# Kernel optimization log

Measured on AMD Instinct MI355X. Metric: run time of the kernel, lower is better.

Reference implementation:

```python
import jax, jax.numpy as jnp
import numpy as np

H = W = 256          # full-res feature map (2h x 2w)
WIN = 16             # window size
STRIDE = 2           # shifted-window stride
HEADS = 8
DIM_HEAD = 64
INNER = HEADS * DIM_HEAD
DIM = 128
KEEP = 50            # min(int(0.7*(256//16)**2), 50)
IOU_THR = 0.2


def _make_windows():
    xs = np.arange(0, W - WIN + 1, STRIDE)
    ys = np.arange(0, H - WIN + 1, STRIDE)
    gx, gy = np.meshgrid(xs, ys)
    return np.stack([gx.ravel(), gy.ravel(), gx.ravel() + WIN - 1, gy.ravel() + WIN - 1], axis=1)

_WIN_NP = _make_windows()          # [M,4] = (x1,y1,x2,y2), M = 121*121 = 14641
BOXES = jnp.asarray(_WIN_NP, dtype=jnp.float32)
SXY = jnp.asarray(_WIN_NP[:, :2], dtype=jnp.int32)   # integer (sx, sy) origins

# torchvision roi_align (spatial_scale=1, sampling_ratio->ceil(15/16)=1, aligned=False):
_off = (np.arange(WIN) + 0.5) * (WIN - 1.0) / WIN
LO = jnp.asarray(np.floor(_off).astype(np.int32))      # low integer index, in [0,14]
FR = jnp.asarray((_off - np.floor(_off)).astype(np.float32))


def _nms_keep(scores):
    """Greedy NMS over the fixed window grid; returns top-KEEP kept indices."""
    x1, y1, x2, y2 = BOXES[:, 0], BOXES[:, 1], BOXES[:, 2], BOXES[:, 3]
    area = (x2 - x1) * (y2 - y1)

    def body(k, carry):
        live, keep = carry
        idx = jnp.argmax(jnp.where(live, scores, -jnp.inf))
        bb = BOXES[idx]
        iw = jnp.clip(jnp.minimum(x2, bb[2]) - jnp.maximum(x1, bb[0]), 0.0)
        ih = jnp.clip(jnp.minimum(y2, bb[3]) - jnp.maximum(y1, bb[1]), 0.0)
        inter = iw * ih
        iou = inter / (area + area[idx] - inter)
        live = live & (iou <= IOU_THR)
        return live, keep.at[k].set(idx.astype(jnp.int32))

    _, keep = jax.lax.fori_loop(
        0, KEEP, body,
        (jnp.ones(BOXES.shape[0], bool), jnp.zeros(KEEP, jnp.int32)))
    return keep


def _forward(x, prob, fix_w, w_qkv, w_out, b_out):
    b = prob.shape[0]
    d = x.shape[-1]
    # entropy map at half res
    entropy = -jnp.sum(prob * jnp.log2(prob + 1e-10), axis=1)          # [b,128,128]
    # FixCNN: 8x8 ones-init conv, VALID -> [b,1,121,121]; normalized window score
    score = jax.lax.conv_general_dilated(
        entropy[:, None], fix_w, (1, 1), 'VALID',
        dimension_numbers=('NCHW', 'OIHW', 'NCHW'))
    score = score.reshape(b, -1) / float((WIN // 2) * (WIN // 2))      # [b,14641]

    keep = jax.lax.stop_gradient(jax.vmap(_nms_keep)(score))           # [b,KEEP]
    sx = SXY[keep][..., 0]                                             # [b,KEEP]
    sy = SXY[keep][..., 1]

    x2d = x.reshape(b, H, W, d)   # token n = h*W + w (channels-last layout)
    ar = jnp.arange(WIN)

    def gather_one(xi, syi, sxi):  # xi [H,W,d]
        R = syi[:, None, None] + ar[None, :, None]
        C = sxi[:, None, None] + ar[None, None, :]
        return xi[R, C]

    crops = jax.vmap(gather_one)(x2d, sy, sx)                          # [b,K,16,16,d]

    # roi_align bilinear sampling with fixed fractional grid
    c00 = crops[:, :, LO[:, None], LO[None, :]]
    c01 = crops[:, :, LO[:, None], LO[None, :] + 1]
    c10 = crops[:, :, LO[:, None] + 1, LO[None, :]]
    c11 = crops[:, :, LO[:, None] + 1, LO[None, :] + 1]
    fy = FR[:, None, None]
    fx = FR[None, :, None]
    win = ((1 - fy) * (1 - fx) * c00 + (1 - fy) * fx * c01
           + fy * (1 - fx) * c10 + fy * fx * c11)                      # [b,K,16,16,d]

    toks = win.reshape(b * KEEP, WIN * WIN, d)                         # [m,256,d]
    qkv = toks @ w_qkv.T                                               # [m,256,3*INNER]
    q, k_, v = jnp.split(qkv, 3, axis=-1)

    def to_heads(t):
        return t.reshape(t.shape[0], t.shape[1], HEADS, DIM_HEAD).transpose(0, 2, 1, 3)

    q, k_, v = to_heads(q), to_heads(k_), to_heads(v)
    attn = jax.nn.softmax(jnp.einsum('mhnd,mhkd->mhnk', q, k_) * (DIM_HEAD ** -0.5), axis=-1)
    out = jnp.einsum('mhnk,mhkd->mhnd', attn, v)
    out = out.transpose(0, 2, 1, 3).reshape(b * KEEP, WIN * WIN, INNER)
    out = out @ w_out.T + b_out                                        # [m,256,d]

    # overlap scatter-add + count normalization
    out2d = out.reshape(b, KEEP, WIN, WIN, d)
    bidx = jnp.arange(b)[:, None, None, None]
    Y = sy[:, :, None, None] + ar[None, None, :, None]
    X = sx[:, :, None, None] + ar[None, None, None, :]
    acc = jnp.zeros((b, H, W, d), x.dtype).at[bidx, Y, X].add(out2d)
    cnt = jnp.zeros((b, H, W), x.dtype).at[bidx, Y, X].add(1.0)
    outx = (acc / (cnt[..., None] + 1e-10)).reshape(b, H * W, d)
    return x + outx


def setup_inputs() -> dict:
    key = jax.random.key(0)
    ks = jax.random.split(key, 4)
    b = 4
    x = jax.random.normal(ks[0], (b, H * W, DIM), dtype=jnp.float32)
    prob = jax.random.uniform(ks[1], (b, 2, H // 2, W // 2), dtype=jnp.float32)
    fix_w = jnp.ones((1, 1, WIN // 2, WIN // 2), dtype=jnp.float32)
    w_qkv = jax.random.normal(ks[2], (3 * INNER, DIM), dtype=jnp.float32) * 0.02
    w_out = jax.random.normal(ks[3], (DIM, INNER), dtype=jnp.float32) * 0.02
    b_out = jnp.zeros((DIM,), dtype=jnp.float32)
    return {"x": x, "prob": prob, "fix_w": fix_w, "w_qkv": w_qkv, "w_out": w_out, "b_out": b_out}


def reference(x, prob, fix_w, w_qkv, w_out, b_out):
    return _forward(x, prob, fix_w, w_qkv, w_out, b_out)
```

## Files before the change

kernel.cpp:

```cpp
#include <hip/hip_runtime.h>
#include <math.h>

#define NB 4
#define NWIN 121
#define NBOX (NWIN*NWIN)
#define NKEEP 50
#define HWD 256
#define DIM 128
#define HEADS 8
#define NTOK 256
#define NWTOT (NB*NKEEP)
#define SCPAD 15616

#define OFF_ENT   0
#define OFF_SCORE 65536
#define OFF_KEEP  128128
#define OFF_WQKV  128256
#define OFF_WOUT  226560
#define OFF_TOKBF 259328
#define OFF_PO    3536128
#define WS_FLOATS 6812928

#define KPAD 76
#define VPAD 268

typedef __attribute__((ext_vector_type(8))) short short8;
typedef __attribute__((ext_vector_type(4))) short short4v;
typedef __attribute__((ext_vector_type(4))) float f32x4;

static __device__ __forceinline__ unsigned short f2bf(float f) {
  union { float f; unsigned u; } v; v.f = f;
  unsigned r = (v.u + 0x7fffu + ((v.u >> 16) & 1u)) >> 16;
  return (unsigned short)r;
}
static __device__ __forceinline__ short4v pk4(f32x4 a) {
  short4v r;
  r[0] = (short)f2bf(a[0]); r[1] = (short)f2bf(a[1]);
  r[2] = (short)f2bf(a[2]); r[3] = (short)f2bf(a[3]);
  return r;
}
static __device__ __forceinline__ short8 ld8_lds(const unsigned short* p) {
  short4v a = *(const short4v*)p;
  short4v b = *(const short4v*)(p + 4);
  short8 r;
  r[0]=a[0]; r[1]=a[1]; r[2]=a[2]; r[3]=a[3];
  r[4]=b[0]; r[5]=b[1]; r[6]=b[2]; r[7]=b[3];
  return r;
}
static __device__ __forceinline__ short8 ld8_g(const unsigned short* p) {
  return *(const short8*)p;
}

template<int CTRL>
static __device__ __forceinline__ float dppmax(float v) {
  union { float f; int i; } a, r; a.f = v;
  r.i = __builtin_amdgcn_update_dpp(a.i, a.i, CTRL, 0xf, 0xf, false);
  return fmaxf(v, r.f);
}
static __device__ __forceinline__ float wavemax(float v) {
  v = dppmax<0x111>(v); v = dppmax<0x112>(v);
  v = dppmax<0x114>(v); v = dppmax<0x118>(v);
  v = dppmax<0x142>(v); v = dppmax<0x143>(v);
  union { float f; int i; } gi, gm; gi.f = v;
  gm.i = __builtin_amdgcn_readlane(gi.i, 63);
  return gm.f;
}

__global__ void k_entropy(const float* __restrict__ prob, float* __restrict__ ent) {
  int idx = blockIdx.x * 256 + threadIdx.x;
  int b = idx >> 14, p = idx & 16383;
  float p0 = prob[(size_t)(b * 2) * 16384 + p];
  float p1 = prob[(size_t)(b * 2 + 1) * 16384 + p];
  ent[idx] = -(p0 * log2f(p0 + 1e-10f) + p1 * log2f(p1 + 1e-10f));
}

__global__ void k_score(const float* __restrict__ ent, const float* __restrict__ fw,
                        float* __restrict__ scp) {
  int gid = blockIdx.x * 256 + threadIdx.x;
  if (gid >= NB * SCPAD) return;
  int b = gid / SCPAD, idx = gid % SCPAD;
  int r = idx >> 7, c = idx & 127;
  float s = -INFINITY;
  if (r < NWIN && c < NWIN) {
    const float* e = ent + b * 16384 + r * 128 + c;
    float a = 0.f;
#pragma unroll
    for (int rr = 0; rr < 8; ++rr)
#pragma unroll
      for (int cc = 0; cc < 8; ++cc)
        a += e[rr * 128 + cc] * fw[rr * 8 + cc];
    s = a * (1.0f / 64.0f);
  }
  scp[b * SCPAD + (r << 7) + (c ^ ((r & 7) << 2))] = s;
}

__global__ void k_nms(const float* __restrict__ scp, int* __restrict__ keep) {
  __shared__ float sc[SCPAD];
  int b = blockIdx.x, l = threadIdx.x;
  const float* src = scp + b * SCPAD;
  for (int cb = 0; cb < 64; cb += 8) {
    f32x4 t[8];
#pragma unroll
    for (int i = 0; i < 8; ++i) {
      int idx = (cb + i) * 256 + l * 4;
      if (idx < SCPAD) t[i] = *(const f32x4*)&src[idx];
    }
#pragma unroll
    for (int i = 0; i < 8; ++i) {
      int idx = (cb + i) * 256 + l * 4;
      if (idx < SCPAD) *(f32x4*)&sc[idx] = t[i];
    }
  }
  float M0 = -INFINITY, M1 = -INFINITY; int C0 = 0, C1 = 0;
#pragma unroll
  for (int slot = 0; slot < 2; ++slot) {
    int r = l + slot * 64;
    if (slot == 1 && r >= NWIN) break;
    int r7 = (r & 7) << 2, rbase = r << 7;
    float bv0=-INFINITY,bv1=-INFINITY,bv2=-INFINITY,bv3=-INFINITY;
    int bc0=0,bc1=0,bc2=0,bc3=0;
    for (int lb = 0; lb < 32; ++lb) {
      f32x4 v = *(const f32x4*)&sc[rbase + ((lb << 2) ^ r7)];
      int c0 = lb << 2;
      if (v[0] > bv0) { bv0 = v[0]; bc0 = c0; }
      if (v[1] > bv1) { bv1 = v[1]; bc1 = c0 + 1; }
      if (v[2] > bv2) { bv2 = v[2]; bc2 = c0 + 2; }
      if (v[3] > bv3) { bv3 = v[3]; bc3 = c0 + 3; }
    }
    float bv = bv0; int bc = bc0;
    if (bv1 > bv || (bv1 == bv && bc1 < bc)) { bv = bv1; bc = bc1; }
    if (bv2 > bv || (bv2 == bv && bc2 < bc)) { bv = bv2; bc = bc2; }
    if (bv3 > bv || (bv3 == bv && bc3 < bc)) { bv = bv3; bc = bc3; }
    if (slot == 0) { M0 = bv; C0 = bc; } else { M1 = bv; C1 = bc; }
  }

  for (int k = 0; k < NKEEP; ++k) {
    float gmax = wavemax(fmaxf(M0, M1));
    unsigned long long b0 = __ballot(M0 == gmax);
    unsigned long long b1 = __ballot(M1 == gmax);
    int R;
    if (b0) R = __ffsll((unsigned long long)b0) - 1;
    else    R = 64 + __ffsll((unsigned long long)b1) - 1;
    int Cc = (R < 64) ? __builtin_amdgcn_readlane(C0, R)
                      : __builtin_amdgcn_readlane(C1, R - 64);
    if (l == 0) {
      keep[(b * NKEEP + k) * 2 + 0] = 2 * R;
      keep[(b * NKEEP + k) * 2 + 1] = 2 * Cc;
    }
    bool kill0 = false, kill1 = false;
    {
      int dy = l - R, ady = dy < 0 ? -dy : dy;
      if (ady <= 4) {
        int ih = 15 - 2 * ady;
#pragma unroll
        for (int dx = -4; dx <= 4; ++dx) {
          int adx = dx < 0 ? -dx : dx;
          if ((15 - 2 * adx) * ih > 75) {
            int cc = Cc + dx;
            if ((unsigned)cc < (unsigned)NWIN)
              sc[(l << 7) + (cc ^ ((l & 7) << 2))] = -INFINITY;
          }
        }
        int adx = C0 - Cc; adx = adx < 0 ? -adx : adx;
        kill0 = (adx <= 4) && ((15 - 2 * adx) * ih > 75);
      }
    }
    if (l + 64 < NWIN) {
      int r1 = l + 64;
      int dy = r1 - R, ady = dy < 0 ? -dy : dy;
      if (ady <= 4) {
        int ih = 15 - 2 * ady;
#pragma unroll
        for (int dx = -4; dx <= 4; ++dx) {
          int adx = dx < 0 ? -dx : dx;
          if ((15 - 2 * adx) * ih > 75) {
            int cc = Cc + dx;
            if ((unsigned)cc < (unsigned)NWIN)
              sc[(r1 << 7) + (cc ^ ((r1 & 7) << 2))] = -INFINITY;
          }
        }
        int adx = C1 - Cc; adx = adx < 0 ? -adx : adx;
        kill1 = (adx <= 4) && ((15 - 2 * adx) * ih > 75);
      }
    }
    unsigned long long need0 = __ballot(kill0);
    unsigned long long need1 = __ballot(kill1);
    while (need0 | need1) {
      int rr;
      if (need0) { rr = __ffsll((unsigned long long)need0) - 1; need0 &= need0 - 1; }
      else       { rr = __ffsll((unsigned long long)need1) - 1 + 64; need1 &= need1 - 1; }
      int r7 = (rr & 7) << 2, rbase = rr << 7;
      float v0 = sc[rbase + (l ^ r7)];
      float v1 = sc[rbase + ((l + 64) ^ r7)];
      float rmax = wavemax(fmaxf(v0, v1));
      unsigned long long e0 = __ballot(v0 == rmax);
      unsigned long long e1 = __ballot(v1 == rmax);
      int bc;
      if (e0) bc = __ffsll((unsigned long long)e0) - 1;
      else    bc = 64 + __ffsll((unsigned long long)e1) - 1;
      if (l == (rr & 63)) {
        if (rr >= 64) { M1 = rmax; C1 = bc; }
        else          { M0 = rmax; C0 = bc; }
      }
    }
  }
}

__global__ void k_wcvt(const float* __restrict__ wqkv, const float* __restrict__ wout,
                       unsigned short* __restrict__ wqkv_bf, unsigned short* __restrict__ wout_bf) {
  int i = blockIdx.x * 256 + threadIdx.x;
  if (i < 196608) wqkv_bf[i] = f2bf(wqkv[i]);
  int j = i - 196608;
  if (j >= 0 && j < 65536) wout_bf[j] = f2bf(wout[j]);
}

__global__ void k_toks(const float* __restrict__ x, const int* __restrict__ keep,
                       unsigned short* __restrict__ tokbf) {
  int w = blockIdx.x;
  int b = w / NKEEP;
  int sy = keep[w * 2 + 0], sx = keep[w * 2 + 1];
  int tid = threadIdx.x;
  int ch = tid & 127, th = tid >> 7;
  const float* xb = x + (size_t)b * 65536 * DIM;
  for (int it = 0; it < 128; ++it) {
    int tk = it * 2 + th;
    int i = tk >> 4, j = tk & 15;
    float offy = (i + 0.5f) * 0.9375f;
    float offx = (j + 0.5f) * 0.9375f;
    int li = (int)offy, lj = (int)offx;
    float fy = offy - (float)li, fx = offx - (float)lj;
    const float* p = xb + ((size_t)((sy + li) * HWD + (sx + lj))) * DIM + ch;
    float v00 = p[0], v01 = p[DIM], v10 = p[HWD * DIM], v11 = p[HWD * DIM + DIM];
    float w00 = (1.f - fy) * (1.f - fx), w01 = (1.f - fy) * fx;
    float w10 = fy * (1.f - fx), w11 = fy * fx;
    tokbf[((size_t)w * NTOK + tk) * DIM + ch] = f2bf(w00 * v00 + w01 * v01 + w10 * v10 + w11 * v11);
  }
}

__global__ __launch_bounds__(512, 2) void k_attn(
    const unsigned short* __restrict__ tokbf,
    const unsigned short* __restrict__ wqkv,
    const unsigned short* __restrict__ wout,
    unsigned short* __restrict__ po) {
  __shared__ __align__(16) char smem[112128];
  unsigned short* Klds = (unsigned short*)smem;
  unsigned short* VT   = (unsigned short*)(smem + 38912);
  const int tid = threadIdx.x;
  const int wv = tid >> 6, ln = tid & 63;
  const int lo = ln & 15, hi = ln >> 4;
  const int win = blockIdx.x;
  unsigned short* QP = (unsigned short*)(smem + 73216 + wv * 4864);
  const unsigned short* tw = tokbf + (size_t)win * NTOK * DIM;
  const int qrow = wv * 32;

  f32x4 pacc[8][2];
#pragma unroll
  for (int mf = 0; mf < 8; ++mf)
#pragma unroll
    for (int nf = 0; nf < 2; ++nf) pacc[mf][nf] = (f32x4){0.f,0.f,0.f,0.f};

  for (int h = 0; h < HEADS; ++h) {
    if (h) __syncthreads();

    {
      f32x4 kacc[4][2];
#pragma unroll
      for (int mf = 0; mf < 4; ++mf)
#pragma unroll
        for (int nf = 0; nf < 2; ++nf) kacc[mf][nf] = (f32x4){0.f,0.f,0.f,0.f};
#pragma unroll
      for (int kf = 0; kf < 4; ++kf) {
        short8 aw[4], bt[2];
#pragma unroll
        for (int mf = 0; mf < 4; ++mf)
          aw[mf] = ld8_g(wqkv + (size_t)(512 + h * 64 + mf * 16 + lo) * 128 + kf * 32 + hi * 8);
#pragma unroll
        for (int nf = 0; nf < 2; ++nf)
          bt[nf] = ld8_g(&tw[(qrow + nf * 16 + lo) * 128 + kf * 32 + hi * 8]);
#pragma unroll
        for (int mf = 0; mf < 4; ++mf)
#pragma unroll
          for (int nf = 0; nf < 2; ++nf)
            kacc[mf][nf] = __builtin_amdgcn_mfma_f32_16x16x32_bf16(aw[mf], bt[nf], kacc[mf][nf], 0, 0, 0);
      }
#pragma unroll
      for (int mf = 0; mf < 4; ++mf)
#pragma unroll
        for (int nf = 0; nf < 2; ++nf)
          *(short4v*)&Klds[(qrow + nf * 16 + lo) * KPAD + mf * 16 + hi * 4] = pk4(kacc[mf][nf]);
    }
    {
      f32x4 vacc[2][4];
#pragma unroll
      for (int mf = 0; mf < 2; ++mf)
#pragma unroll
        for (int nf = 0; nf < 4; ++nf) vacc[mf][nf] = (f32x4){0.f,0.f,0.f,0.f};
#pragma unroll
      for (int kf = 0; kf < 4; ++kf) {
        short8 at[2], bw[4];
#pragma unroll
        for (int mf = 0; mf < 2; ++mf)
          at[mf] = ld8_g(&tw[(qrow + mf * 16 + lo) * 128 + kf * 32 + hi * 8]);
#pragma unroll
        for (int nf = 0; nf < 4; ++nf)
          bw[nf] = ld8_g(wqkv + (size_t)(1024 + h * 64 + nf * 16 + lo) * 128 + kf * 32 + hi * 8);
#pragma unroll
        for (int mf = 0; mf < 2; ++mf)
#pragma unroll
          for (int nf = 0; nf < 4; ++nf)
            vacc[mf][nf] = __builtin_amdgcn_mfma_f32_16x16x32_bf16(at[mf], bw[nf], vacc[mf][nf], 0, 0, 0);
      }
#pragma unroll
      for (int mf = 0; mf < 2; ++mf)
#pragma unroll
        for (int nf = 0; nf < 4; ++nf)
          *(short4v*)&VT[(nf * 16 + lo) * VPAD + qrow + mf * 16 + hi * 4] = pk4(vacc[mf][nf]);
    }
    {
      f32x4 qacc[4][2];
#pragma unroll
      for (int mf = 0; mf < 4; ++mf)
#pragma unroll
        for (int nf = 0; nf < 2; ++nf) qacc[mf][nf] = (f32x4){0.f,0.f,0.f,0.f};
#pragma unroll
      for (int kf = 0; kf < 4; ++kf) {
        short8 aw[4], bt[2];
#pragma unroll
        for (int mf = 0; mf < 4; ++mf)
          aw[mf] = ld8_g(wqkv + (size_t)(h * 64 + mf * 16 + lo) * 128 + kf * 32 + hi * 8);
#pragma unroll
        for (int nf = 0; nf < 2; ++nf)
          bt[nf] = ld8_g(&tw[(qrow + nf * 16 + lo) * 128 + kf * 32 + hi * 8]);
#pragma unroll
        for (int mf = 0; mf < 4; ++mf)
#pragma unroll
          for (int nf = 0; nf < 2; ++nf)
            qacc[mf][nf] = __builtin_amdgcn_mfma_f32_16x16x32_bf16(aw[mf], bt[nf], qacc[mf][nf], 0, 0, 0);
      }
#pragma unroll
      for (int mf = 0; mf < 4; ++mf)
#pragma unroll
        for (int nf = 0; nf < 2; ++nf)
          *(short4v*)&QP[(nf * 16 + lo) * KPAD + mf * 16 + hi * 4] = pk4(qacc[mf][nf] * 0.125f);
    }
    __syncthreads();

    short8 Qb[2][2];
#pragma unroll
    for (int nf = 0; nf < 2; ++nf)
#pragma unroll
      for (int kf = 0; kf < 2; ++kf)
        Qb[nf][kf] = ld8_lds(&QP[(nf * 16 + lo) * KPAD + kf * 32 + hi * 8]);

    f32x4 Ot[4][2];
#pragma unroll
    for (int mf = 0; mf < 4; ++mf)
#pragma unroll
      for (int nf = 0; nf < 2; ++nf) Ot[mf][nf] = (f32x4){0.f,0.f,0.f,0.f};
    float mrow[2] = {-INFINITY, -INFINITY};
    float lrow[2] = {0.f, 0.f};

    for (int ck = 0; ck < 4; ++ck) {
      f32x4 sacc[4][2];
#pragma unroll
      for (int mf = 0; mf < 4; ++mf)
#pragma unroll
        for (int nf = 0; nf < 2; ++nf) sacc[mf][nf] = (f32x4){0.f,0.f,0.f,0.f};
      short8 ka[4][2];
#pragma unroll
      for (int mf = 0; mf < 4; ++mf)
#pragma unroll
        for (int kf = 0; kf < 2; ++kf)
          ka[mf][kf] = ld8_lds(&Klds[(ck * 64 + mf * 16 + lo) * KPAD + kf * 32 + hi * 8]);
#pragma unroll
      for (int mf = 0; mf < 4; ++mf)
#pragma unroll
        for (int nf = 0; nf < 2; ++nf)
#pragma unroll
          for (int kf = 0; kf < 2; ++kf)
            sacc[mf][nf] = __builtin_amdgcn_mfma_f32_16x16x32_bf16(ka[mf][kf], Qb[nf][kf], sacc[mf][nf], 0, 0, 0);

#pragma unroll
      for (int nf = 0; nf < 2; ++nf) {
        float cmax = -INFINITY;
#pragma unroll
        for (int mf = 0; mf < 4; ++mf)
#pragma unroll
          for (int r = 0; r < 4; ++r) cmax = fmaxf(cmax, sacc[mf][nf][r]);
        cmax = fmaxf(cmax, __shfl_xor(cmax, 16));
        cmax = fmaxf(cmax, __shfl_xor(cmax, 32));
        float mnew = fmaxf(mrow[nf], cmax);
        float corr = __expf(mrow[nf] - mnew);
        float ps = 0.f;
#pragma unroll
        for (int mf = 0; mf < 4; ++mf)
#pragma unroll
          for (int r = 0; r < 4; ++r) {
            float e = __expf(sacc[mf][nf][r] - mnew);
            sacc[mf][nf][r] = e; ps += e;
          }
        ps += __shfl_xor(ps, 16);
        ps += __shfl_xor(ps, 32);
        lrow[nf] = lrow[nf] * corr + ps;
        mrow[nf] = mnew;
#pragma unroll
        for (int mf = 0; mf < 4; ++mf) Ot[mf][nf] *= corr;
      }
#pragma unroll
      for (int mf = 0; mf < 4; ++mf)
#pragma unroll
        for (int nf = 0; nf < 2; ++nf)
          *(short4v*)&QP[(nf * 16 + lo) * KPAD + mf * 16 + hi * 4] = pk4(sacc[mf][nf]);
      short8 pb[2][2], va[4][2];
#pragma unroll
      for (int nf = 0; nf < 2; ++nf)
#pragma unroll
        for (int kf = 0; kf < 2; ++kf)
          pb[nf][kf] = ld8_lds(&QP[(nf * 16 + lo) * KPAD + kf * 32 + hi * 8]);
#pragma unroll
      for (int mf = 0; mf < 4; ++mf)
#pragma unroll
        for (int kf = 0; kf < 2; ++kf)
          va[mf][kf] = ld8_lds(&VT[(mf * 16 + lo) * VPAD + ck * 64 + kf * 32 + hi * 8]);
#pragma unroll
      for (int mf = 0; mf < 4; ++mf)
#pragma unroll
        for (int nf = 0; nf < 2; ++nf)
#pragma unroll
          for (int kf = 0; kf < 2; ++kf)
            Ot[mf][nf] = __builtin_amdgcn_mfma_f32_16x16x32_bf16(va[mf][kf], pb[nf][kf], Ot[mf][nf], 0, 0, 0);
    }

#pragma unroll
    for (int nf = 0; nf < 2; ++nf) {
      float inv = 1.f / lrow[nf];
#pragma unroll
      for (int mf = 0; mf < 4; ++mf)
        *(short4v*)&QP[(nf * 16 + lo) * KPAD + mf * 16 + hi * 4] = pk4(Ot[mf][nf] * inv);
    }
    short8 Ob[2][2];
#pragma unroll
    for (int nf = 0; nf < 2; ++nf)
#pragma unroll
      for (int kf = 0; kf < 2; ++kf)
        Ob[nf][kf] = ld8_lds(&QP[(nf * 16 + lo) * KPAD + kf * 32 + hi * 8]);
#pragma unroll
    for (int kf = 0; kf < 2; ++kf) {
      short8 aw[8];
#pragma unroll
      for (int mf = 0; mf < 8; ++mf)
        aw[mf] = ld8_g(wout + (size_t)(mf * 16 + lo) * 512 + h * 64 + kf * 32 + hi * 8);
#pragma unroll
      for (int mf = 0; mf < 8; ++mf)
#pragma unroll
        for (int nf = 0; nf < 2; ++nf)
          pacc[mf][nf] = __builtin_amdgcn_mfma_f32_16x16x32_bf16(aw[mf], Ob[nf][kf], pacc[mf][nf], 0, 0, 0);
    }
  }

#pragma unroll
  for (int mf = 0; mf < 8; ++mf)
#pragma unroll
    for (int nf = 0; nf < 2; ++nf)
      *(short4v*)&po[((size_t)win * NTOK + qrow + nf * 16 + lo) * 128 + mf * 16 + hi * 4] = pk4(pacc[mf][nf]);
}

__global__ void k_final(const float* __restrict__ x, const unsigned short* __restrict__ po,
                        const int* __restrict__ keep, const float* __restrict__ bout,
                        float* __restrict__ out) {
  __shared__ int kp[2 * NKEEP];
  int tid = threadIdx.x;
  int gid = blockIdx.x * 256 + tid;
  int chq = gid & 3, pix = gid >> 2;
  int b = pix >> 16, pb = pix & 65535, y = pb >> 8, xx = pb & 255;
  if (tid < 2 * NKEEP) kp[tid] = keep[b * 2 * NKEEP + tid];
  __syncthreads();
  float acc[32];
#pragma unroll
  for (int i = 0; i < 32; ++i) acc[i] = 0.f;
  float cnt = 0.f;
  for (int w = 0; w < NKEEP; ++w) {
    int dy = y - kp[2 * w], dx = xx - kp[2 * w + 1];
    if ((unsigned)dy < 16u && (unsigned)dx < 16u) {
      cnt += 1.f;
      const unsigned short* pp = po + ((size_t)(b * NKEEP + w) * NTOK + dy * 16 + dx) * 128 + chq * 32;
#pragma unroll
      for (int k2 = 0; k2 < 4; ++k2) {
        short8 v = ld8_g(pp + k2 * 8);
#pragma unroll
        for (int j = 0; j < 8; ++j) {
          union { unsigned u; float f; } cv;
          cv.u = ((unsigned)(unsigned short)v[j]) << 16;
          acc[k2 * 8 + j] += cv.f;
        }
      }
    }
  }
  size_t base = (size_t)pix * 128 + chq * 32;
  float inv = 1.f / (cnt + 1e-10f);
#pragma unroll
  for (int i = 0; i < 32; ++i)
    out[base + i] = x[base + i] + (acc[i] + cnt * bout[chq * 32 + i]) * inv;
}

extern "C" void kernel_launch(void* const* d_in, const int* in_sizes, int n_in,
                              void* d_out, int out_size, void* d_ws, size_t ws_size,
                              hipStream_t stream) {
  const float* x    = (const float*)d_in[0];
  const float* prob = (const float*)d_in[1];
  const float* fixw = (const float*)d_in[2];
  const float* wqkv = (const float*)d_in[3];
  const float* wout = (const float*)d_in[4];
  const float* bout = (const float*)d_in[5];
  float* out = (float*)d_out;
  float* ws  = (float*)d_ws;
  if (ws_size < WS_FLOATS * sizeof(float)) return;

  float* ent  = ws + OFF_ENT;
  float* scp  = ws + OFF_SCORE;
  int*   keep = (int*)(ws + OFF_KEEP);
  unsigned short* wqkv_bf = (unsigned short*)(ws + OFF_WQKV);
  unsigned short* wout_bf = (unsigned short*)(ws + OFF_WOUT);
  unsigned short* tokbf   = (unsigned short*)(ws + OFF_TOKBF);
  unsigned short* po      = (unsigned short*)(ws + OFF_PO);

  k_entropy<<<256, 256, 0, stream>>>(prob, ent);
  k_score<<<(NB * SCPAD + 255) / 256, 256, 0, stream>>>(ent, fixw, scp);
  k_wcvt<<<1024, 256, 0, stream>>>(wqkv, wout, wqkv_bf, wout_bf);
  k_nms<<<NB, 64, 0, stream>>>(scp, keep);
  k_toks<<<NWTOT, 256, 0, stream>>>(x, keep, tokbf);
  k_attn<<<NWTOT, 512, 0, stream>>>(tokbf, wqkv_bf, wout_bf, po);
  k_final<<<NB * 65536 * 4 / 256, 256, 0, stream>>>(x, po, keep, bout, out);
}
```

Baseline: 390.2 us.

## Split fused window attention into per-head K/V, flash, and projection kernels

```diff
diff --git a/kernel.cpp b/kernel.cpp
--- a/kernel.cpp
+++ b/kernel.cpp
@@ -19,7 +19,8 @@
 #define OFF_WOUT  226560
 #define OFF_TOKBF 259328
 #define OFF_PO    3536128
-#define WS_FLOATS 6812928
+#define WS_SMALL  6812928
+#define OFF_KG    6812928
 
 #define KPAD 76
 #define VPAD 268
@@ -133,7 +134,6 @@
     if (bv3 > bv || (bv3 == bv && bc3 < bc)) { bv = bv3; bc = bc3; }
     if (slot == 0) { M0 = bv; C0 = bc; } else { M1 = bv; C1 = bc; }
   }
-
   for (int k = 0; k < NKEEP; ++k) {
     float gmax = wavemax(fmaxf(M0, M1));
     unsigned long long b0 = __ballot(M0 == gmax);
@@ -237,6 +237,254 @@
   }
 }
 
+
+__global__ __launch_bounds__(256, 2) void k_kv(
+    const unsigned short* __restrict__ tokbf,
+    const unsigned short* __restrict__ wqkv,
+    unsigned short* __restrict__ Kg,
+    unsigned short* __restrict__ VTg, int win0) {
+  int bid = blockIdx.x;
+  int win = win0 + (bid >> 3), h = bid & 7;
+  int tid = threadIdx.x;
+  int wv = tid >> 6, ln = tid & 63, lo = ln & 15, hi = ln >> 4;
+  const unsigned short* tw = tokbf + (size_t)win * NTOK * DIM;
+  int kb = wv * 64;
+  unsigned short* Kb = Kg + (size_t)bid * 16384;
+  unsigned short* Vb = VTg + (size_t)bid * 16384;
+  {
+    f32x4 kacc[4][4];
+#pragma unroll
+    for (int mf = 0; mf < 4; ++mf)
+#pragma unroll
+      for (int nf = 0; nf < 4; ++nf) kacc[mf][nf] = (f32x4){0.f,0.f,0.f,0.f};
+#pragma unroll
+    for (int kf = 0; kf < 4; ++kf) {
+      short8 aw[4], bt[4];
+#pragma unroll
+      for (int mf = 0; mf < 4; ++mf)
+        aw[mf] = ld8_g(wqkv + (size_t)(512 + h * 64 + mf * 16 + lo) * 128 + kf * 32 + hi * 8);
+#pragma unroll
+      for (int nf = 0; nf < 4; ++nf)
+        bt[nf] = ld8_g(&tw[(kb + nf * 16 + lo) * 128 + kf * 32 + hi * 8]);
+#pragma unroll
+      for (int mf = 0; mf < 4; ++mf)
+#pragma unroll
+        for (int nf = 0; nf < 4; ++nf)
+          kacc[mf][nf] = __builtin_amdgcn_mfma_f32_16x16x32_bf16(aw[mf], bt[nf], kacc[mf][nf], 0, 0, 0);
+    }
+#pragma unroll
+    for (int mf = 0; mf < 4; ++mf)
+#pragma unroll
+      for (int nf = 0; nf < 4; ++nf)
+        *(short4v*)&Kb[(kb + nf * 16 + lo) * 64 + mf * 16 + hi * 4] = pk4(kacc[mf][nf]);
+  }
+  {
+    f32x4 vacc[4][4];
+#pragma unroll
+    for (int mf = 0; mf < 4; ++mf)
+#pragma unroll
+      for (int nf = 0; nf < 4; ++nf) vacc[mf][nf] = (f32x4){0.f,0.f,0.f,0.f};
+#pragma unroll
+    for (int kf = 0; kf < 4; ++kf) {
+      short8 at[4], bw[4];
+#pragma unroll
+      for (int mf = 0; mf < 4; ++mf)
+        at[mf] = ld8_g(&tw[(kb + mf * 16 + lo) * 128 + kf * 32 + hi * 8]);
+#pragma unroll
+      for (int nf = 0; nf < 4; ++nf)
+        bw[nf] = ld8_g(wqkv + (size_t)(1024 + h * 64 + nf * 16 + lo) * 128 + kf * 32 + hi * 8);
+#pragma unroll
+      for (int mf = 0; mf < 4; ++mf)
+#pragma unroll
+        for (int nf = 0; nf < 4; ++nf)
+          vacc[mf][nf] = __builtin_amdgcn_mfma_f32_16x16x32_bf16(at[mf], bw[nf], vacc[mf][nf], 0, 0, 0);
+    }
+#pragma unroll
+    for (int mf = 0; mf < 4; ++mf)
+#pragma unroll
+      for (int nf = 0; nf < 4; ++nf)
+        *(short4v*)&Vb[(nf * 16 + lo) * 256 + kb + mf * 16 + hi * 4] = pk4(vacc[mf][nf]);
+  }
+}
+
+__global__ __launch_bounds__(512, 2) void k_flash(
+    const unsigned short* __restrict__ tokbf,
+    const unsigned short* __restrict__ wqkv,
+    const unsigned short* __restrict__ Kg,
+    const unsigned short* __restrict__ VTg,
+    unsigned short* __restrict__ Oall, int win0) {
+  __shared__ unsigned short QPall[8 * 2176];
+  int bid = blockIdx.x;
+  int lw = bid >> 3, h = bid & 7;
+  int win = win0 + lw;
+  int tid = threadIdx.x;
+  int wv = tid >> 6, ln = tid & 63, lo = ln & 15, hi = ln >> 4;
+  unsigned short* QP = QPall + wv * 2176;
+  const unsigned short* tw = tokbf + (size_t)win * NTOK * DIM;
+  const unsigned short* Kb = Kg + (size_t)bid * 16384;
+  const unsigned short* Vb = VTg + (size_t)bid * 16384;
+  int qb = wv * 32;
+
+  {
+    f32x4 qacc[4][2];
+#pragma unroll
+    for (int mf = 0; mf < 4; ++mf)
+#pragma unroll
+      for (int nf = 0; nf < 2; ++nf) qacc[mf][nf] = (f32x4){0.f,0.f,0.f,0.f};
+#pragma unroll
+    for (int kf = 0; kf < 4; ++kf) {
+      short8 aw[4], bt[2];
+#pragma unroll
+      for (int mf = 0; mf < 4; ++mf)
+        aw[mf] = ld8_g(wqkv + (size_t)(h * 64 + mf * 16 + lo) * 128 + kf * 32 + hi * 8);
+#pragma unroll
+      for (int nf = 0; nf < 2; ++nf)
+        bt[nf] = ld8_g(&tw[(qb + nf * 16 + lo) * 128 + kf * 32 + hi * 8]);
+#pragma unroll
+      for (int mf = 0; mf < 4; ++mf)
+#pragma unroll
+        for (int nf = 0; nf < 2; ++nf)
+          qacc[mf][nf] = __builtin_amdgcn_mfma_f32_16x16x32_bf16(aw[mf], bt[nf], qacc[mf][nf], 0, 0, 0);
+    }
+#pragma unroll
+    for (int mf = 0; mf < 4; ++mf)
+#pragma unroll
+      for (int nf = 0; nf < 2; ++nf)
+        *(short4v*)&QP[(nf * 16 + lo) * 68 + mf * 16 + hi * 4] = pk4(qacc[mf][nf] * 0.125f);
+  }
+  short8 Qb[2][2];
+#pragma unroll
+  for (int nf = 0; nf < 2; ++nf)
+#pragma unroll
+    for (int kf = 0; kf < 2; ++kf)
+      Qb[nf][kf] = ld8_lds(&QP[(nf * 16 + lo) * 68 + kf * 32 + hi * 8]);
+
+  f32x4 Ot[4][2];
+#pragma unroll
+  for (int mf = 0; mf < 4; ++mf)
+#pragma unroll
+    for (int nf = 0; nf < 2; ++nf) Ot[mf][nf] = (f32x4){0.f,0.f,0.f,0.f};
+  float mrow[2] = {-INFINITY, -INFINITY};
+  float lrow[2] = {0.f, 0.f};
+
+  for (int ck = 0; ck < 4; ++ck) {
+    f32x4 sacc[4][2];
+#pragma unroll
+    for (int mf = 0; mf < 4; ++mf)
+#pragma unroll
+      for (int nf = 0; nf < 2; ++nf) sacc[mf][nf] = (f32x4){0.f,0.f,0.f,0.f};
+    short8 ka[4][2];
+#pragma unroll
+    for (int mf = 0; mf < 4; ++mf)
+#pragma unroll
+      for (int kf = 0; kf < 2; ++kf)
+        ka[mf][kf] = ld8_g(&Kb[(ck * 64 + mf * 16 + lo) * 64 + kf * 32 + hi * 8]);
+#pragma unroll
+    for (int mf = 0; mf < 4; ++mf)
+#pragma unroll
+      for (int nf = 0; nf < 2; ++nf)
+#pragma unroll
+        for (int kf = 0; kf < 2; ++kf)
+          sacc[mf][nf] = __builtin_amdgcn_mfma_f32_16x16x32_bf16(ka[mf][kf], Qb[nf][kf], sacc[mf][nf], 0, 0, 0);
+
+#pragma unroll
+    for (int nf = 0; nf < 2; ++nf) {
+      float cmax = -INFINITY;
+#pragma unroll
+      for (int mf = 0; mf < 4; ++mf)
+#pragma unroll
+        for (int r = 0; r < 4; ++r) cmax = fmaxf(cmax, sacc[mf][nf][r]);
+      cmax = fmaxf(cmax, __shfl_xor(cmax, 16));
+      cmax = fmaxf(cmax, __shfl_xor(cmax, 32));
+      float mnew = fmaxf(mrow[nf], cmax);
+      float corr = __expf(mrow[nf] - mnew);
+      float ps = 0.f;
+#pragma unroll
+      for (int mf = 0; mf < 4; ++mf)
+#pragma unroll
+        for (int r = 0; r < 4; ++r) {
+          float e = __expf(sacc[mf][nf][r] - mnew);
+          sacc[mf][nf][r] = e; ps += e;
+        }
+      ps += __shfl_xor(ps, 16);
+      ps += __shfl_xor(ps, 32);
+      lrow[nf] = lrow[nf] * corr + ps;
+      mrow[nf] = mnew;
+#pragma unroll
+      for (int mf = 0; mf < 4; ++mf) Ot[mf][nf] *= corr;
+    }
+#pragma unroll
+    for (int mf = 0; mf < 4; ++mf)
+#pragma unroll
+      for (int nf = 0; nf < 2; ++nf)
+        *(short4v*)&QP[(nf * 16 + lo) * 68 + mf * 16 + hi * 4] = pk4(sacc[mf][nf]);
+    short8 pb[2][2], va[4][2];
+#pragma unroll
+    for (int nf = 0; nf < 2; ++nf)
+#pragma unroll
+      for (int kf = 0; kf < 2; ++kf)
+        pb[nf][kf] = ld8_lds(&QP[(nf * 16 + lo) * 68 + kf * 32 + hi * 8]);
+#pragma unroll
+    for (int mf = 0; mf < 4; ++mf)
+#pragma unroll
+      for (int kf = 0; kf < 2; ++kf)
+        va[mf][kf] = ld8_g(&Vb[(mf * 16 + lo) * 256 + ck * 64 + kf * 32 + hi * 8]);
+#pragma unroll
+    for (int mf = 0; mf < 4; ++mf)
+#pragma unroll
+      for (int nf = 0; nf < 2; ++nf)
+#pragma unroll
+        for (int kf = 0; kf < 2; ++kf)
+          Ot[mf][nf] = __builtin_amdgcn_mfma_f32_16x16x32_bf16(va[mf][kf], pb[nf][kf], Ot[mf][nf], 0, 0, 0);
+  }
+#pragma unroll
+  for (int nf = 0; nf < 2; ++nf) {
+    float inv = 1.f / lrow[nf];
+#pragma unroll
+    for (int mf = 0; mf < 4; ++mf)
+      *(short4v*)&Oall[((size_t)lw * 256 + qb + nf * 16 + lo) * 512 + h * 64 + mf * 16 + hi * 4]
+        = pk4(Ot[mf][nf] * inv);
+  }
+}
+
+__global__ __launch_bounds__(512, 2) void k_proj(
+    const unsigned short* __restrict__ Oall,
+    const unsigned short* __restrict__ wout,
+    unsigned short* __restrict__ po, int win0) {
+  int lw = blockIdx.x;
+  int win = win0 + lw;
+  int tid = threadIdx.x;
+  int wv = tid >> 6, ln = tid & 63, lo = ln & 15, hi = ln >> 4;
+  int qb = wv * 32;
+  const unsigned short* Ob = Oall + (size_t)lw * 131072;
+  f32x4 pacc[8][2];
+#pragma unroll
+  for (int mf = 0; mf < 8; ++mf)
+#pragma unroll
+    for (int nf = 0; nf < 2; ++nf) pacc[mf][nf] = (f32x4){0.f,0.f,0.f,0.f};
+#pragma unroll
+  for (int kf = 0; kf < 16; ++kf) {
+    short8 aw[8], bt[2];
+#pragma unroll
+    for (int mf = 0; mf < 8; ++mf)
+      aw[mf] = ld8_g(wout + (size_t)(mf * 16 + lo) * 512 + kf * 32 + hi * 8);
+#pragma unroll
+    for (int nf = 0; nf < 2; ++nf)
+      bt[nf] = ld8_g(&Ob[(qb + nf * 16 + lo) * 512 + kf * 32 + hi * 8]);
+#pragma unroll
+    for (int mf = 0; mf < 8; ++mf)
+#pragma unroll
+      for (int nf = 0; nf < 2; ++nf)
+        pacc[mf][nf] = __builtin_amdgcn_mfma_f32_16x16x32_bf16(aw[mf], bt[nf], pacc[mf][nf], 0, 0, 0);
+  }
+#pragma unroll
+  for (int mf = 0; mf < 8; ++mf)
+#pragma unroll
+    for (int nf = 0; nf < 2; ++nf)
+      *(short4v*)&po[((size_t)win * NTOK + qb + nf * 16 + lo) * 128 + mf * 16 + hi * 4]
+        = pk4(pacc[mf][nf]);
+}
+
 __global__ __launch_bounds__(512, 2) void k_attn(
     const unsigned short* __restrict__ tokbf,
     const unsigned short* __restrict__ wqkv,
@@ -261,7 +509,6 @@
 
   for (int h = 0; h < HEADS; ++h) {
     if (h) __syncthreads();
-
     {
       f32x4 kacc[4][2];
 #pragma unroll
@@ -457,7 +704,6 @@
           pacc[mf][nf] = __builtin_amdgcn_mfma_f32_16x16x32_bf16(aw[mf], Ob[nf][kf], pacc[mf][nf], 0, 0, 0);
     }
   }
-
 #pragma unroll
   for (int mf = 0; mf < 8; ++mf)
 #pragma unroll
@@ -514,7 +760,7 @@
   const float* bout = (const float*)d_in[5];
   float* out = (float*)d_out;
   float* ws  = (float*)d_ws;
-  if (ws_size < WS_FLOATS * sizeof(float)) return;
+  if (ws_size < (size_t)WS_SMALL * 4) return;
 
   float* ent  = ws + OFF_ENT;
   float* scp  = ws + OFF_SCORE;
@@ -524,11 +770,28 @@
   unsigned short* tokbf   = (unsigned short*)(ws + OFF_TOKBF);
   unsigned short* po      = (unsigned short*)(ws + OFF_PO);
 
+  int W = 0;
+  if      (ws_size >= ((size_t)OFF_KG + 3ULL * 200 * 65536) * 4) W = 200;
+  else if (ws_size >= ((size_t)OFF_KG + 3ULL * 100 * 65536) * 4) W = 100;
+  else if (ws_size >= ((size_t)OFF_KG + 3ULL *  50 * 65536) * 4) W = 50;
+
   k_entropy<<<256, 256, 0, stream>>>(prob, ent);
   k_score<<<(NB * SCPAD + 255) / 256, 256, 0, stream>>>(ent, fixw, scp);
   k_wcvt<<<1024, 256, 0, stream>>>(wqkv, wout, wqkv_bf, wout_bf);
   k_nms<<<NB, 64, 0, stream>>>(scp, keep);
   k_toks<<<NWTOT, 256, 0, stream>>>(x, keep, tokbf);
-  k_attn<<<NWTOT, 512, 0, stream>>>(tokbf, wqkv_bf, wout_bf, po);
+
+  if (W > 0) {
+    unsigned short* Kg   = (unsigned short*)(ws + OFF_KG);
+    unsigned short* VTg  = (unsigned short*)(ws + OFF_KG + (size_t)W * 65536);
+    unsigned short* Oall = (unsigned short*)(ws + OFF_KG + (size_t)W * 131072);
+    for (int win0 = 0; win0 < NWTOT; win0 += W) {
+      k_kv<<<W * 8, 256, 0, stream>>>(tokbf, wqkv_bf, Kg, VTg, win0);
+      k_flash<<<W * 8, 512, 0, stream>>>(tokbf, wqkv_bf, Kg, VTg, Oall, win0);
+      k_proj<<<W, 512, 0, stream>>>(Oall, wout_bf, po, win0);
+    }
+  } else {
+    k_attn<<<NWTOT, 512, 0, stream>>>(tokbf, wqkv_bf, wout_bf, po);
+  }
   k_final<<<NB * 65536 * 4 / 256, 256, 0, stream>>>(x, po, keep, bout, out);
 }
```

Result: slower. 491.6 us (+26.0%).

## Split attention per window into two query-half blocks with half-sized K/V staging

Applied to the files above, without the earlier changes.

```diff
diff --git a/kernel.cpp b/kernel.cpp
--- a/kernel.cpp
+++ b/kernel.cpp
@@ -21,8 +21,8 @@
 #define OFF_PO    3536128
 #define WS_FLOATS 6812928
 
-#define KPAD 76
-#define VPAD 268
+#define KP3 68
+#define VP3 132
 
 typedef __attribute__((ext_vector_type(8))) short short8;
 typedef __attribute__((ext_vector_type(4))) short short4v;
@@ -133,7 +133,6 @@
     if (bv3 > bv || (bv3 == bv && bc3 < bc)) { bv = bv3; bc = bc3; }
     if (slot == 0) { M0 = bv; C0 = bc; } else { M1 = bv; C1 = bc; }
   }
-
   for (int k = 0; k < NKEEP; ++k) {
     float gmax = wavemax(fmaxf(M0, M1));
     unsigned long long b0 = __ballot(M0 == gmax);
@@ -237,213 +236,169 @@
   }
 }
 
-__global__ __launch_bounds__(512, 2) void k_attn(
+__global__ __launch_bounds__(512, 4) void k_attn3(
     const unsigned short* __restrict__ tokbf,
     const unsigned short* __restrict__ wqkv,
     const unsigned short* __restrict__ wout,
     unsigned short* __restrict__ po) {
-  __shared__ __align__(16) char smem[112128];
-  unsigned short* Klds = (unsigned short*)smem;
-  unsigned short* VT   = (unsigned short*)(smem + 38912);
+  __shared__ __align__(16) char smem[51712];
+  unsigned short* Kh  = (unsigned short*)smem;
+  unsigned short* VTh = (unsigned short*)(smem + 17408);
   const int tid = threadIdx.x;
-  const int wv = tid >> 6, ln = tid & 63;
-  const int lo = ln & 15, hi = ln >> 4;
-  const int win = blockIdx.x;
-  unsigned short* QP = (unsigned short*)(smem + 73216 + wv * 4864);
+  const int wv = tid >> 6, ln = tid & 63, lo = ln & 15, hi = ln >> 4;
+  const int bid = blockIdx.x;
+  const int win = bid >> 1, qh = bid & 1;
+  unsigned short* QP = (unsigned short*)(smem + 34304 + wv * 2176);
   const unsigned short* tw = tokbf + (size_t)win * NTOK * DIM;
-  const int qrow = wv * 32;
-
-  f32x4 pacc[8][2];
-#pragma unroll
-  for (int mf = 0; mf < 8; ++mf)
-#pragma unroll
-    for (int nf = 0; nf < 2; ++nf) pacc[mf][nf] = (f32x4){0.f,0.f,0.f,0.f};
+  const int qb = qh * 128 + wv * 16;
+
+  f32x4 pacc[8];
+#pragma unroll
+  for (int mf = 0; mf < 8; ++mf) pacc[mf] = (f32x4){0.f,0.f,0.f,0.f};
 
   for (int h = 0; h < HEADS; ++h) {
-    if (h) __syncthreads();
-
     {
-      f32x4 kacc[4][2];
+      f32x4 qacc[4];
+#pragma unroll
+      for (int mf = 0; mf < 4; ++mf) qacc[mf] = (f32x4){0.f,0.f,0.f,0.f};
+#pragma unroll
+      for (int kf = 0; kf < 4; ++kf) {
+        short8 aw[4], bt;
+#pragma unroll
+        for (int mf = 0; mf < 4; ++mf)
+          aw[mf] = ld8_g(wqkv + (size_t)(h * 64 + mf * 16 + lo) * 128 + kf * 32 + hi * 8);
+        bt = ld8_g(&tw[(qb + lo) * 128 + kf * 32 + hi * 8]);
+#pragma unroll
+        for (int mf = 0; mf < 4; ++mf)
+          qacc[mf] = __builtin_amdgcn_mfma_f32_16x16x32_bf16(aw[mf], bt, qacc[mf], 0, 0, 0);
+      }
 #pragma unroll
       for (int mf = 0; mf < 4; ++mf)
-#pragma unroll
-        for (int nf = 0; nf < 2; ++nf) kacc[mf][nf] = (f32x4){0.f,0.f,0.f,0.f};
-#pragma unroll
-      for (int kf = 0; kf < 4; ++kf) {
-        short8 aw[4], bt[2];
-#pragma unroll
-        for (int mf = 0; mf < 4; ++mf)
-          aw[mf] = ld8_g(wqkv + (size_t)(512 + h * 64 + mf * 16 + lo) * 128 + kf * 32 + hi * 8);
-#pragma unroll
-        for (int nf = 0; nf < 2; ++nf)
-          bt[nf] = ld8_g(&tw[(qrow + nf * 16 + lo) * 128 + kf * 32 + hi * 8]);
-#pragma unroll
-        for (int mf = 0; mf < 4; ++mf)
-#pragma unroll
-          for (int nf = 0; nf < 2; ++nf)
-            kacc[mf][nf] = __builtin_amdgcn_mfma_f32_16x16x32_bf16(aw[mf], bt[nf], kacc[mf][nf], 0, 0, 0);
-      }
-#pragma unroll
-      for (int mf = 0; mf < 4; ++mf)
-#pragma unroll
-        for (int nf = 0; nf < 2; ++nf)
-          *(short4v*)&Klds[(qrow + nf * 16 + lo) * KPAD + mf * 16 + hi * 4] = pk4(kacc[mf][nf]);
-    }
-    {
-      f32x4 vacc[2][4];
-#pragma unroll
-      for (int mf = 0; mf < 2; ++mf)
-#pragma unroll
-        for (int nf = 0; nf < 4; ++nf) vacc[mf][nf] = (f32x4){0.f,0.f,0.f,0.f};
-#pragma unroll
-      for (int kf = 0; kf < 4; ++kf) {
-        short8 at[2], bw[4];
-#pragma unroll
-        for (int mf = 0; mf < 2; ++mf)
-          at[mf] = ld8_g(&tw[(qrow + mf * 16 + lo) * 128 + kf * 32 + hi * 8]);
+        *(short4v*)&QP[lo * KP3 + mf * 16 + hi * 4] = pk4(qacc[mf] * 0.125f);
+    }
+    short8 Qb[2];
+#pragma unroll
+    for (int kf = 0; kf < 2; ++kf)
+      Qb[kf] = ld8_lds(&QP[lo * KP3 + kf * 32 + hi * 8]);
+
+    f32x4 Ot[4];
+#pragma unroll
+    for (int mf = 0; mf < 4; ++mf) Ot[mf] = (f32x4){0.f,0.f,0.f,0.f};
+    float mrow = -INFINITY, lrow = 0.f;
+
+    for (int half = 0; half < 2; ++half) {
+      __syncthreads();
+      const int kbase = half * 128 + wv * 16;
+      {
+        f32x4 kacc[4];
+#pragma unroll
+        for (int mf = 0; mf < 4; ++mf) kacc[mf] = (f32x4){0.f,0.f,0.f,0.f};
+#pragma unroll
+        for (int kf = 0; kf < 4; ++kf) {
+          short8 aw[4], bt;
+#pragma unroll
+          for (int mf = 0; mf < 4; ++mf)
+            aw[mf] = ld8_g(wqkv + (size_t)(512 + h * 64 + mf * 16 + lo) * 128 + kf * 32 + hi * 8);
+          bt = ld8_g(&tw[(kbase + lo) * 128 + kf * 32 + hi * 8]);
+#pragma unroll
+          for (int mf = 0; mf < 4; ++mf)
+            kacc[mf] = __builtin_amdgcn_mfma_f32_16x16x32_bf16(aw[mf], bt, kacc[mf], 0, 0, 0);
+        }
+#pragma unroll
+        for (int mf = 0; mf < 4; ++mf)
+          *(short4v*)&Kh[(wv * 16 + lo) * KP3 + mf * 16 + hi * 4] = pk4(kacc[mf]);
+      }
+      {
+        f32x4 vacc[4];
+#pragma unroll
+        for (int nf = 0; nf < 4; ++nf) vacc[nf] = (f32x4){0.f,0.f,0.f,0.f};
+#pragma unroll
+        for (int kf = 0; kf < 4; ++kf) {
+          short8 at, bw[4];
+          at = ld8_g(&tw[(kbase + lo) * 128 + kf * 32 + hi * 8]);
+#pragma unroll
+          for (int nf = 0; nf < 4; ++nf)
+            bw[nf] = ld8_g(wqkv + (size_t)(1024 + h * 64 + nf * 16 + lo) * 128 + kf * 32 + hi * 8);
+#pragma unroll
+          for (int nf = 0; nf < 4; ++nf)
+            vacc[nf] = __builtin_amdgcn_mfma_f32_16x16x32_bf16(at, bw[nf], vacc[nf], 0, 0, 0);
+        }
 #pragma unroll
         for (int nf = 0; nf < 4; ++nf)
-          bw[nf] = ld8_g(wqkv + (size_t)(1024 + h * 64 + nf * 16 + lo) * 128 + kf * 32 + hi * 8);
-#pragma unroll
-        for (int mf = 0; mf < 2; ++mf)
-#pragma unroll
-          for (int nf = 0; nf < 4; ++nf)
-            vacc[mf][nf] = __builtin_amdgcn_mfma_f32_16x16x32_bf16(at[mf], bw[nf], vacc[mf][nf], 0, 0, 0);
-      }
-#pragma unroll
-      for (int mf = 0; mf < 2; ++mf)
-#pragma unroll
-        for (int nf = 0; nf < 4; ++nf)
-          *(short4v*)&VT[(nf * 16 + lo) * VPAD + qrow + mf * 16 + hi * 4] = pk4(vacc[mf][nf]);
-    }
-    {
-      f32x4 qacc[4][2];
-#pragma unroll
-      for (int mf = 0; mf < 4; ++mf)
-#pragma unroll
-        for (int nf = 0; nf < 2; ++nf) qacc[mf][nf] = (f32x4){0.f,0.f,0.f,0.f};
-#pragma unroll
-      for (int kf = 0; kf < 4; ++kf) {
-        short8 aw[4], bt[2];
-#pragma unroll
-        for (int mf = 0; mf < 4; ++mf)
-          aw[mf] = ld8_g(wqkv + (size_t)(h * 64 + mf * 16 + lo) * 128 + kf * 32 + hi * 8);
-#pragma unroll
-        for (int nf = 0; nf < 2; ++nf)
-          bt[nf] = ld8_g(&tw[(qrow + nf * 16 + lo) * 128 + kf * 32 + hi * 8]);
-#pragma unroll
-        for (int mf = 0; mf < 4; ++mf)
-#pragma unroll
-          for (int nf = 0; nf < 2; ++nf)
-            qacc[mf][nf] = __builtin_amdgcn_mfma_f32_16x16x32_bf16(aw[mf], bt[nf], qacc[mf][nf], 0, 0, 0);
-      }
-#pragma unroll
-      for (int mf = 0; mf < 4; ++mf)
-#pragma unroll
-        for (int nf = 0; nf < 2; ++nf)
-          *(short4v*)&QP[(nf * 16 + lo) * KPAD + mf * 16 + hi * 4] = pk4(qacc[mf][nf] * 0.125f);
-    }
-    __syncthreads();
-
-    short8 Qb[2][2];
-#pragma unroll
-    for (int nf = 0; nf < 2; ++nf)
-#pragma unroll
-      for (int kf = 0; kf < 2; ++kf)
-        Qb[nf][kf] = ld8_lds(&QP[(nf * 16 + lo) * KPAD + kf * 32 + hi * 8]);
-
-    f32x4 Ot[4][2];
-#pragma unroll
-    for (int mf = 0; mf < 4; ++mf)
-#pragma unroll
-      for (int nf = 0; nf < 2; ++nf) Ot[mf][nf] = (f32x4){0.f,0.f,0.f,0.f};
-    float mrow[2] = {-INFINITY, -INFINITY};
-    float lrow[2] = {0.f, 0.f};
-
-    for (int ck = 0; ck < 4; ++ck) {
-      f32x4 sacc[4][2];
-#pragma unroll
-      for (int mf = 0; mf < 4; ++mf)
-#pragma unroll
-        for (int nf = 0; nf < 2; ++nf) sacc[mf][nf] = (f32x4){0.f,0.f,0.f,0.f};
-      short8 ka[4][2];
-#pragma unroll
-      for (int mf = 0; mf < 4; ++mf)
-#pragma unroll
-        for (int kf = 0; kf < 2; ++kf)
-          ka[mf][kf] = ld8_lds(&Klds[(ck * 64 + mf * 16 + lo) * KPAD + kf * 32 + hi * 8]);
-#pragma unroll
-      for (int mf = 0; mf < 4; ++mf)
-#pragma unroll
-        for (int nf = 0; nf < 2; ++nf)
+          *(short4v*)&VTh[(nf * 16 + lo) * VP3 + wv * 16 + hi * 4] = pk4(vacc[nf]);
+      }
+      __syncthreads();
+
+      for (int ck = 0; ck < 2; ++ck) {
+        f32x4 sacc[4];
+#pragma unroll
+        for (int mf = 0; mf < 4; ++mf) sacc[mf] = (f32x4){0.f,0.f,0.f,0.f};
+        short8 ka[4][2];
+#pragma unroll
+        for (int mf = 0; mf < 4; ++mf)
 #pragma unroll
           for (int kf = 0; kf < 2; ++kf)
-            sacc[mf][nf] = __builtin_amdgcn_mfma_f32_16x16x32_bf16(ka[mf][kf], Qb[nf][kf], sacc[mf][nf], 0, 0, 0);
-
-#pragma unroll
-      for (int nf = 0; nf < 2; ++nf) {
+            ka[mf][kf] = ld8_lds(&Kh[(ck * 64 + mf * 16 + lo) * KP3 + kf * 32 + hi * 8]);
+#pragma unroll
+        for (int mf = 0; mf < 4; ++mf)
+#pragma unroll
+          for (int kf = 0; kf < 2; ++kf)
+            sacc[mf] = __builtin_amdgcn_mfma_f32_16x16x32_bf16(ka[mf][kf], Qb[kf], sacc[mf], 0, 0, 0);
+
         float cmax = -INFINITY;
 #pragma unroll
         for (int mf = 0; mf < 4; ++mf)
 #pragma unroll
-          for (int r = 0; r < 4; ++r) cmax = fmaxf(cmax, sacc[mf][nf][r]);
+          for (int r = 0; r < 4; ++r) cmax = fmaxf(cmax, sacc[mf][r]);
         cmax = fmaxf(cmax, __shfl_xor(cmax, 16));
         cmax = fmaxf(cmax, __shfl_xor(cmax, 32));
-        float mnew = fmaxf(mrow[nf], cmax);
-        float corr = __expf(mrow[nf] - mnew);
+        float mnew = fmaxf(mrow, cmax);
+        float corr = __expf(mrow - mnew);
         float ps = 0.f;
 #pragma unroll
         for (int mf = 0; mf < 4; ++mf)
 #pragma unroll
           for (int r = 0; r < 4; ++r) {
-            float e = __expf(sacc[mf][nf][r] - mnew);
-            sacc[mf][nf][r] = e; ps += e;
+            float e = __expf(sacc[mf][r] - mnew);
+            sacc[mf][r] = e; ps += e;
           }
         ps += __shfl_xor(ps, 16);
         ps += __shfl_xor(ps, 32);
-        lrow[nf] = lrow[nf] * corr + ps;
-        mrow[nf] = mnew;
-#pragma unroll
-        for (int mf = 0; mf < 4; ++mf) Ot[mf][nf] *= corr;
-      }
+        lrow = lrow * corr + ps;
+        mrow = mnew;
+#pragma unroll
+        for (int mf = 0; mf < 4; ++mf) Ot[mf] *= corr;
+
+#pragma unroll
+        for (int mf = 0; mf < 4; ++mf)
+          *(short4v*)&QP[lo * KP3 + mf * 16 + hi * 4] = pk4(sacc[mf]);
+        short8 pb[2], va[4][2];
+#pragma unroll
+        for (int kf = 0; kf < 2; ++kf)
+          pb[kf] = ld8_lds(&QP[lo * KP3 + kf * 32 + hi * 8]);
+#pragma unroll
+        for (int mf = 0; mf < 4; ++mf)
+#pragma unroll
+          for (int kf = 0; kf < 2; ++kf)
+            va[mf][kf] = ld8_lds(&VTh[(mf * 16 + lo) * VP3 + ck * 64 + kf * 32 + hi * 8]);
+#pragma unroll
+        for (int mf = 0; mf < 4; ++mf)
+#pragma unroll
+          for (int kf = 0; kf < 2; ++kf)
+            Ot[mf] = __builtin_amdgcn_mfma_f32_16x16x32_bf16(va[mf][kf], pb[kf], Ot[mf], 0, 0, 0);
+      }
+    }
+
+    {
+      float inv = 1.f / lrow;
 #pragma unroll
       for (int mf = 0; mf < 4; ++mf)
-#pragma unroll
-        for (int nf = 0; nf < 2; ++nf)
-          *(short4v*)&QP[(nf * 16 + lo) * KPAD + mf * 16 + hi * 4] = pk4(sacc[mf][nf]);
-      short8 pb[2][2], va[4][2];
-#pragma unroll
-      for (int nf = 0; nf < 2; ++nf)
-#pragma unroll
-        for (int kf = 0; kf < 2; ++kf)
-          pb[nf][kf] = ld8_lds(&QP[(nf * 16 + lo) * KPAD + kf * 32 + hi * 8]);
-#pragma unroll
-      for (int mf = 0; mf < 4; ++mf)
-#pragma unroll
-        for (int kf = 0; kf < 2; ++kf)
-          va[mf][kf] = ld8_lds(&VT[(mf * 16 + lo) * VPAD + ck * 64 + kf * 32 + hi * 8]);
-#pragma unroll
-      for (int mf = 0; mf < 4; ++mf)
-#pragma unroll
-        for (int nf = 0; nf < 2; ++nf)
-#pragma unroll
-          for (int kf = 0; kf < 2; ++kf)
-            Ot[mf][nf] = __builtin_amdgcn_mfma_f32_16x16x32_bf16(va[mf][kf], pb[nf][kf], Ot[mf][nf], 0, 0, 0);
-    }
-
-#pragma unroll
-    for (int nf = 0; nf < 2; ++nf) {
-      float inv = 1.f / lrow[nf];
-#pragma unroll
-      for (int mf = 0; mf < 4; ++mf)
-        *(short4v*)&QP[(nf * 16 + lo) * KPAD + mf * 16 + hi * 4] = pk4(Ot[mf][nf] * inv);
-    }
-    short8 Ob[2][2];
-#pragma unroll
-    for (int nf = 0; nf < 2; ++nf)
-#pragma unroll
-      for (int kf = 0; kf < 2; ++kf)
-        Ob[nf][kf] = ld8_lds(&QP[(nf * 16 + lo) * KPAD + kf * 32 + hi * 8]);
+        *(short4v*)&QP[lo * KP3 + mf * 16 + hi * 4] = pk4(Ot[mf] * inv);
+    }
+    short8 Ob[2];
+#pragma unroll
+    for (int kf = 0; kf < 2; ++kf)
+      Ob[kf] = ld8_lds(&QP[lo * KP3 + kf * 32 + hi * 8]);
 #pragma unroll
     for (int kf = 0; kf < 2; ++kf) {
       short8 aw[8];
@@ -452,17 +407,13 @@
         aw[mf] = ld8_g(wout + (size_t)(mf * 16 + lo) * 512 + h * 64 + kf * 32 + hi * 8);
 #pragma unroll
       for (int mf = 0; mf < 8; ++mf)
-#pragma unroll
-        for (int nf = 0; nf < 2; ++nf)
-          pacc[mf][nf] = __builtin_amdgcn_mfma_f32_16x16x32_bf16(aw[mf], Ob[nf][kf], pacc[mf][nf], 0, 0, 0);
+        pacc[mf] = __builtin_amdgcn_mfma_f32_16x16x32_bf16(aw[mf], Ob[kf], pacc[mf], 0, 0, 0);
     }
   }
 
 #pragma unroll
   for (int mf = 0; mf < 8; ++mf)
-#pragma unroll
-    for (int nf = 0; nf < 2; ++nf)
-      *(short4v*)&po[((size_t)win * NTOK + qrow + nf * 16 + lo) * 128 + mf * 16 + hi * 4] = pk4(pacc[mf][nf]);
+    *(short4v*)&po[((size_t)win * NTOK + qb + lo) * 128 + mf * 16 + hi * 4] = pk4(pacc[mf]);
 }
 
 __global__ void k_final(const float* __restrict__ x, const unsigned short* __restrict__ po,
@@ -514,7 +465,7 @@
   const float* bout = (const float*)d_in[5];
   float* out = (float*)d_out;
   float* ws  = (float*)d_ws;
-  if (ws_size < WS_FLOATS * sizeof(float)) return;
+  if (ws_size < (size_t)WS_FLOATS * 4) return;
 
   float* ent  = ws + OFF_ENT;
   float* scp  = ws + OFF_SCORE;
@@ -529,6 +480,6 @@
   k_wcvt<<<1024, 256, 0, stream>>>(wqkv, wout, wqkv_bf, wout_bf);
   k_nms<<<NB, 64, 0, stream>>>(scp, keep);
   k_toks<<<NWTOT, 256, 0, stream>>>(x, keep, tokbf);
-  k_attn<<<NWTOT, 512, 0, stream>>>(tokbf, wqkv_bf, wout_bf, po);
+  k_attn3<<<NWTOT * 2, 512, 0, stream>>>(tokbf, wqkv_bf, wout_bf, po);
   k_final<<<NB * 65536 * 4 / 256, 256, 0, stream>>>(x, po, keep, bout, out);
 }
```

After: 800.9 us. 105% more time.
